# Optimization experiments

Hardware: AMD Instinct MI355X
Metric: run time of the kernel (lower is better)

The kernel has to match this reference:

```python
import jax, jax.numpy as jnp
import numpy as np

N = 100000
E = 1000000
C = 64      # hidden_channels
H = 4       # heads
O = C // H  # out channels per head
NEG_SLOPE = 0.2


def setup_inputs() -> dict:
    key = jax.random.key(0)
    ks = jax.random.split(key, 14)
    x = jax.random.normal(ks[0], (N, C), dtype=jnp.float32)
    edge_index = jax.random.randint(ks[1], (2, E), 0, N, dtype=jnp.int64)
    s = 1.0 / np.sqrt(C)
    params = {}
    for l in range(3):
        params[f"Wl{l+1}"] = jax.random.normal(ks[2 + 4 * l], (C, H * O), dtype=jnp.float32) * s
        params[f"Wr{l+1}"] = jax.random.normal(ks[3 + 4 * l], (C, H * O), dtype=jnp.float32) * s
        params[f"a{l+1}"] = jax.random.normal(ks[4 + 4 * l], (H, O), dtype=jnp.float32) * s
        params[f"b{l+1}"] = jnp.zeros((H * O,), dtype=jnp.float32)
    return {"x": x, "edge_index": edge_index, **params}


def _gatv2_layer(x, src, dst, Wl, Wr, a, b):
    # x: [N, C]; src/dst: [E]
    xl = (x @ Wl).reshape(N, H, O)  # source-side transform
    xr = (x @ Wr).reshape(N, H, O)  # target-side transform
    s = jax.nn.leaky_relu(xl[src] + xr[dst], NEG_SLOPE)     # [E, H, O]
    e = jnp.einsum("eho,ho->eh", s, a)                       # [E, H] logits
    # segment softmax over incoming edges of each target node
    m = jax.ops.segment_max(e, dst, num_segments=N)          # [N, H]
    ex = jnp.exp(e - m[dst])
    denom = jax.ops.segment_sum(ex, dst, num_segments=N)     # [N, H]
    alpha = ex / (denom[dst] + 1e-16)                        # [E, H]
    out = jax.ops.segment_sum(xl[src] * alpha[:, :, None], dst, num_segments=N)
    return out.reshape(N, H * O) + b


def reference(x, edge_index, Wl1, Wr1, a1, b1, Wl2, Wr2, a2, b2, Wl3, Wr3, a3, b3):
    src, dst = edge_index[0], edge_index[1]
    h = jax.nn.relu(_gatv2_layer(x, src, dst, Wl1, Wr1, a1, b1))
    h = jax.nn.relu(_gatv2_layer(h, src, dst, Wl2, Wr2, a2, b2))
    h = _gatv2_layer(h, src, dst, Wl3, Wr3, a3, b3)
    return h
```

## Files before the change

### kernel.cpp

```cpp
#include <hip/hip_runtime.h>
#include <hip/hip_fp16.h>
#include <math.h>

#define SLOPE 0.2f
#define LOG2E 1.4426950408889634f

#define DPP_ADD(x, ctrl) \
    ((x) + __int_as_float(__builtin_amdgcn_update_dpp( \
        0, __float_as_int(x), (ctrl), 0xF, 0xF, true)))


#define NPB 256
#define EPB 2048
#define MAXBK 2048

__global__ __launch_bounds__(256) void kH1(const int* __restrict__ ei,
                                           int* __restrict__ hist,
                                           int E, int nbk, int nblkE) {
    __shared__ int h[MAXBK];
    int t = threadIdx.x, b = blockIdx.x;
    for (int i = t; i < nbk; i += 256) h[i] = 0;
    __syncthreads();
    int e0 = b * EPB, e1 = min(e0 + EPB, E);
    for (int e = e0 + t; e < e1; e += 256)
        atomicAdd(&h[ei[E + e] >> 8], 1);
    __syncthreads();
    for (int i = t; i < nbk; i += 256)
        hist[i * nblkE + b] = h[i];
}

__global__ __launch_bounds__(256) void k_scan1(const int* __restrict__ deg,
                                               int* __restrict__ rp,
                                               int* __restrict__ blk, int n) {
    __shared__ int sd[256];
    int t = threadIdx.x;
    int base = blockIdx.x * 1024 + t * 4;
    int v0 = 0, v1 = 0, v2 = 0, v3 = 0;
    if (base + 0 < n) v0 = deg[base + 0];
    if (base + 1 < n) v1 = deg[base + 1];
    if (base + 2 < n) v2 = deg[base + 2];
    if (base + 3 < n) v3 = deg[base + 3];
    int s = v0 + v1 + v2 + v3;
    sd[t] = s;
    __syncthreads();
    for (int off = 1; off < 256; off <<= 1) {
        int x = (t >= off) ? sd[t - off] : 0;
        __syncthreads();
        sd[t] += x;
        __syncthreads();
    }
    int ex = sd[t] - s;
    if (t == 255) blk[blockIdx.x] = sd[255];
    if (base + 0 < n) rp[base + 0] = ex; ex += v0;
    if (base + 1 < n) rp[base + 1] = ex; ex += v1;
    if (base + 2 < n) rp[base + 2] = ex; ex += v2;
    if (base + 3 < n) rp[base + 3] = ex;
}

__global__ __launch_bounds__(256) void k_scan3(int* __restrict__ rp,
                                               const int* __restrict__ blk,
                                               int n) {
    __shared__ int red[256];
    int t = threadIdx.x, b = blockIdx.x;
    int v = 0;
    for (int i = t; i < b; i += 256) v += blk[i];
    red[t] = v;
    __syncthreads();
    for (int off = 128; off; off >>= 1) {
        if (t < off) red[t] += red[t + off];
        __syncthreads();
    }
    int off0 = red[0];
    int base = b * 1024 + t * 4;
    #pragma unroll
    for (int i = 0; i < 4; i++) {
        int idx = base + i;
        if (idx < n) rp[idx] += off0;
    }
}

__global__ __launch_bounds__(256) void kH2(const int* __restrict__ ei,
                                           const int* __restrict__ hs,
                                           int* __restrict__ pairs,
                                           int E, int nbk, int nblkE) {
    __shared__ int soff[MAXBK];
    int t = threadIdx.x, b = blockIdx.x;
    for (int i = t; i < nbk; i += 256) soff[i] = hs[i * nblkE + b];
    __syncthreads();
    int e0 = b * EPB, e1 = min(e0 + EPB, E);
    for (int e = e0 + t; e < e1; e += 256) {
        int s = ei[e], d = ei[E + e];
        int slot = atomicAdd(&soff[d >> 8], 1);
        pairs[slot] = (s << 8) | (d & (NPB - 1));
    }
}

__global__ __launch_bounds__(256) void kB3(const int* __restrict__ hs,
                                           const int* __restrict__ pairs,
                                           int* __restrict__ btot,
                                           int E, int nbk, int nblkE) {
    __shared__ int sdeg[NPB];
    __shared__ int red[256];
    int t = threadIdx.x, b = blockIdx.x;
    sdeg[t] = 0;
    __syncthreads();
    int s0 = hs[b * nblkE];
    int s1 = (b + 1 < nbk) ? hs[(b + 1) * nblkE] : E;
    for (int i = s0 + t; i < s1; i += 256)
        atomicAdd(&sdeg[pairs[i] & (NPB - 1)], 1);
    __syncthreads();
    red[t] = (sdeg[t] + 15) & ~15;
    __syncthreads();
    for (int off = 128; off; off >>= 1) {
        if (t < off) red[t] += red[t + off];
        __syncthreads();
    }
    if (t == 0) btot[b] = red[0];
}

__global__ __launch_bounds__(256) void kB4(const int* __restrict__ hs,
                                           const int* __restrict__ pairs,
                                           const int* __restrict__ btot,
                                           int* __restrict__ rp,
                                           int* __restrict__ deg,
                                           int* __restrict__ col,
                                           int E, int nbk, int nblkE, int n) {
    __shared__ int sdeg[NPB];
    __shared__ int spfx[NPB];
    int t = threadIdx.x, b = blockIdx.x;

    int v = 0;
    for (int i = t; i < b; i += 256) v += btot[i];
    spfx[t] = v;
    __syncthreads();
    for (int off = 128; off; off >>= 1) {
        if (t < off) spfx[t] += spfx[t + off];
        __syncthreads();
    }
    int bb = spfx[0];
    __syncthreads();

    sdeg[t] = 0;
    __syncthreads();
    int s0 = hs[b * nblkE];
    int s1 = (b + 1 < nbk) ? hs[(b + 1) * nblkE] : E;
    for (int i = s0 + t; i < s1; i += 256)
        atomicAdd(&sdeg[pairs[i] & (NPB - 1)], 1);
    __syncthreads();
    int cnt = sdeg[t];
    int pv = (cnt + 15) & ~15;
    spfx[t] = pv;
    __syncthreads();
    for (int off = 1; off < 256; off <<= 1) {
        int x = (t >= off) ? spfx[t - off] : 0;
        __syncthreads();
        spfx[t] += x;
        __syncthreads();
    }
    int rpt = bb + spfx[t] - pv;
    int node = b * NPB + t;
    if (node < n) { rp[node] = rpt; deg[node] = cnt; }
    __syncthreads();
    sdeg[t] = rpt;
    __syncthreads();
    for (int i = s0 + t; i < s1; i += 256) {
        int p = pairs[i];
        int slot = atomicAdd(&sdeg[p & (NPB - 1)], 1);
        col[slot] = (p & ~(NPB - 1)) >> 1;
    }
    if (node < n)
        for (int i = rpt + cnt; i < rpt + pv; i++) col[i] = 0;
}


__global__ __launch_bounds__(512) void k_gemm(const float* __restrict__ in,
                                              const float* __restrict__ Wl,
                                              const float* __restrict__ Wr,
                                              __half* __restrict__ xl,
                                              __half* __restrict__ xr, int n) {
    __shared__ float4 sW[64 * 32];
    __shared__ float  sx[128 * 68];

    int t = threadIdx.x;
    int base = blockIdx.x * 128;

    float4 xs[4];
    int xrow[4], xkq[4];
    #pragma unroll
    for (int s = 0; s < 4; s++) {
        int i = t + 512 * s;
        int row = i >> 4, kq = i & 15;
        int g = base + row;
        if (g > n - 1) g = n - 1;
        xs[s] = *(const float4*)(in + (size_t)g * 64 + kq * 4);
        xrow[s] = row; xkq[s] = kq;
    }
    for (int i = t; i < 2048; i += 512) {
        int k = i >> 5, jg = i & 31;
        const float* src = (jg < 16) ? (Wl + k * 64 + jg * 4)
                                     : (Wr + k * 64 + (jg - 16) * 4);
        sW[i] = *(const float4*)src;
    }
    #pragma unroll
    for (int s = 0; s < 4; s++)
        *(float4*)(sx + xrow[s] * 68 + xkq[s] * 4) = xs[s];
    __syncthreads();

    int rt = t & 31;
    int ct = t >> 5;
    const float* sxp = sx + rt * 68;

    float4 acc[4][2];
    #pragma unroll
    for (int r = 0; r < 4; r++)
        #pragma unroll
        for (int j = 0; j < 2; j++) acc[r][j] = make_float4(0.f, 0.f, 0.f, 0.f);

    #pragma unroll 1
    for (int k0 = 0; k0 < 64; k0 += 4) {
        float4 xv[4];
        #pragma unroll
        for (int r = 0; r < 4; r++)
            xv[r] = *(const float4*)(sxp + r * (32 * 68) + k0);
        #pragma unroll
        for (int kk = 0; kk < 4; kk++) {
            float4 w0 = sW[(k0 + kk) * 32 + ct * 2 + 0];
            float4 w1 = sW[(k0 + kk) * 32 + ct * 2 + 1];
            #pragma unroll
            for (int r = 0; r < 4; r++) {
                float xk = (kk == 0) ? xv[r].x : (kk == 1) ? xv[r].y
                         : (kk == 2) ? xv[r].z : xv[r].w;
                acc[r][0].x += xk * w0.x;
                acc[r][0].y += xk * w0.y;
                acc[r][0].z += xk * w0.z;
                acc[r][0].w += xk * w0.w;
                acc[r][1].x += xk * w1.x;
                acc[r][1].y += xk * w1.y;
                acc[r][1].z += xk * w1.z;
                acc[r][1].w += xk * w1.w;
            }
        }
    }

    __half* outh = (ct < 8) ? xl : xr;
    int cq = (ct & 7) * 8;
    #pragma unroll
    for (int r = 0; r < 4; r++) {
        int g = base + rt + 32 * r;
        if (g < n) {
            union { int4 i4; __half2 h[4]; } u;
            u.h[0] = __floats2half2_rn(acc[r][0].x, acc[r][0].y);
            u.h[1] = __floats2half2_rn(acc[r][0].z, acc[r][0].w);
            u.h[2] = __floats2half2_rn(acc[r][1].x, acc[r][1].y);
            u.h[3] = __floats2half2_rn(acc[r][1].z, acc[r][1].w);
            *(int4*)(outh + (size_t)g * 64 + cq) = u.i4;
        }
    }
}


__global__ __launch_bounds__(256) void k_node(const __half* __restrict__ xl,
                                              const __half* __restrict__ xr,
                                              const int* __restrict__ rp,
                                              const int* __restrict__ deg,
                                              const int* __restrict__ col,
                                              const float* __restrict__ A,
                                              const float* __restrict__ Bv,
                                              float* __restrict__ outp,
                                              int n, int relu) {
    int lane = threadIdx.x & 63;
    int node = __builtin_amdgcn_readfirstlane(blockIdx.x * 4 + (threadIdx.x >> 6));
    if (node >= n) return;
    int grp = lane >> 5;
    int s   = lane & 31;
    int chn = ((s >> 3) << 4) + ((s & 7) << 1);
    unsigned cofs = (unsigned)chn * 2u;

    float2 xr2 = __half22float2(*(const __half2*)(xr + (size_t)node * 64 + chn));
    float2 a2  = *(const float2*)(A + chn);
    a2.x *= LOG2E; a2.y *= LOG2E;
    float2 b2  = *(const float2*)(Bv + chn);

    int start = rp[node];
    int d = deg[node];
    int nb = (d + 7) >> 3;
    const int* cp = col + start;
    const char* xlb = (const char*)xl;

    float den = 0.f;
    float ax = 0.f, ay = 0.f;

    auto batch = [&](const float2 (&v)[4], int ebase, bool full) {
        #pragma unroll
        for (int j = 0; j < 4; j++) {
            float sx_ = v[j].x + xr2.x;
            float sy_ = v[j].y + xr2.y;
            sx_ = fmaxf(sx_, SLOPE * sx_);
            sy_ = fmaxf(sy_, SLOPE * sy_);
            float q = sx_ * a2.x + sy_ * a2.y;
            q = DPP_ADD(q, 0xB1);
            q = DPP_ADD(q, 0x4E);
            q = DPP_ADD(q, 0x141);
            if (!full) {
                int eidx = ebase + 2 * j + grp;
                if (eidx >= d) q = -INFINITY;
            }
            float w = __builtin_amdgcn_exp2f(q);
            den += w;
            ax += w * v[j].x;
            ay += w * v[j].y;
        }
    };

    auto gather = [&](float2 (&v)[4], const int* q) {
        int c[8];
        *(int4*)(c + 0) = *(const int4*)(q + 0);
        *(int4*)(c + 4) = *(const int4*)(q + 4);
        #pragma unroll
        for (int j = 0; j < 4; j++) {
            unsigned cc = (unsigned)(grp ? c[2 * j + 1] : c[2 * j]);
            v[j] = __half22float2(*(const __half2*)(xlb + (cc + cofs)));
        }
    };

    float2 v[4];
    if (nb > 0) gather(v, cp);

    #pragma unroll 1
    for (int b = 0; b < nb - 1; b++) {
        float2 vN[4];
        gather(vN, cp + (b + 1) * 8);
        batch(v, b * 8, true);
        #pragma unroll
        for (int j = 0; j < 4; j++) v[j] = vN[j];
    }
    if (nb > 0) batch(v, (nb - 1) * 8, false);

    den += __shfl_xor(den, 32, 64);
    ax  += __shfl_xor(ax, 32, 64);
    ay  += __shfl_xor(ay, 32, 64);

    float inv = 1.f / (den + 1e-16f);
    float ox = ax * inv + b2.x;
    float oy = ay * inv + b2.y;
    if (relu) { ox = fmaxf(ox, 0.f); oy = fmaxf(oy, 0.f); }
    if (grp == 0)
        *(float2*)(outp + (size_t)node * 64 + chn) = make_float2(ox, oy);
}


extern "C" void kernel_launch(void* const* d_in, const int* in_sizes, int n_in,
                              void* d_out, int out_size, void* d_ws, size_t ws_size,
                              hipStream_t stream) {
    const float* x = (const float*)d_in[0];
    const int* ei = (const int*)d_in[1];
    int N = in_sizes[0] / 64;
    int E = in_sizes[1] / 2;

    const float* Wl[3] = {(const float*)d_in[2], (const float*)d_in[6], (const float*)d_in[10]};
    const float* Wr[3] = {(const float*)d_in[3], (const float*)d_in[7], (const float*)d_in[11]};
    const float* Av[3] = {(const float*)d_in[4], (const float*)d_in[8], (const float*)d_in[12]};
    const float* Bv[3] = {(const float*)d_in[5], (const float*)d_in[9], (const float*)d_in[13]};

    char* w = (char*)d_ws;
    auto carve = [&](size_t bytes) {
        void* p = (void*)w;
        w += (bytes + 255) & ~(size_t)255;
        return p;
    };
    int NBK    = (N + NPB - 1) / NPB;
    int NBLK_E = (E + EPB - 1) / EPB;
    size_t histN = (size_t)NBK * NBLK_E;
    size_t colN = (size_t)E + 15 * (size_t)N + 64;
    __half* xl   = (__half*)carve((size_t)N * 64 * 2);
    __half* xr   = (__half*)carve((size_t)N * 64 * 2);
    float* h     = (float*)carve((size_t)N * 64 * 4);
    int*   rp    = (int*)carve((size_t)N * 4);
    int*   deg   = (int*)carve((size_t)N * 4);
    int*   col   = (int*)carve(colN * 4);
    int*   pairs = (int*)carve((size_t)E * 4);
    int*   hist  = (int*)carve(histN * 4);
    int*   hs    = (int*)carve(histN * 4);
    int*   btot  = (int*)carve((size_t)NBK * 4);
    int*   blkB  = (int*)carve(512 * 4);

    int nblkH1024 = (int)((histN + 1023) / 1024);
    int gemm_grid = (N + 127) / 128;
    int node_grid = (N + 3) / 4;

    kH1<<<NBLK_E, 256, 0, stream>>>(ei, hist, E, NBK, NBLK_E);
    k_scan1<<<nblkH1024, 256, 0, stream>>>(hist, hs, blkB, (int)histN);
    k_scan3<<<nblkH1024, 256, 0, stream>>>(hs, blkB, (int)histN);
    kH2<<<NBLK_E, 256, 0, stream>>>(ei, hs, pairs, E, NBK, NBLK_E);

    kB3<<<NBK, 256, 0, stream>>>(hs, pairs, btot, E, NBK, NBLK_E);
    kB4<<<NBK, 256, 0, stream>>>(hs, pairs, btot, rp, deg, col, E, NBK, NBLK_E, N);

    const float* in_l = x;
    for (int l = 0; l < 3; l++) {
        float* out_l = (l == 2) ? (float*)d_out : h;
        int relu = (l < 2) ? 1 : 0;
        k_gemm<<<gemm_grid, 512, 0, stream>>>(in_l, Wl[l], Wr[l], xl, xr, N);
        k_node<<<node_grid, 256, 0, stream>>>(xl, xr, rp, deg, col, Av[l], Bv[l],
                                              out_l, N, relu);
        in_l = h;
    }
}
```

Measured before the change: 325.9 us.

## Fuse node aggregation with next layer's GEMM via shared memory

Adds a k_fused kernel that runs the edge-softmax aggregation for 128 nodes per block, applies bias and ReLU, keeps the 64-channel result in shared memory, and then multiplies it by the next layer's Wl and Wr to write the fp16 xl and xr directly. Layers 1 and 2 use this kernel with ping-pong buffers, so the fp32 hidden tensor is never written to or read back from global memory and two launches are dropped. The cost is lower parallelism per block: each wave now handles 16 nodes one after another with half-wave edge batches, where k_node used many small blocks, and the larger shared-memory footprint may reduce occupancy.

```diff
diff --git a/kernel.cpp b/kernel.cpp
--- a/kernel.cpp
+++ b/kernel.cpp
@@ -243,6 +243,166 @@
     }
 
     __half* outh = (ct < 8) ? xl : xr;
+    int cq = (ct & 7) * 8;
+    #pragma unroll
+    for (int r = 0; r < 4; r++) {
+        int g = base + rt + 32 * r;
+        if (g < n) {
+            union { int4 i4; __half2 h[4]; } u;
+            u.h[0] = __floats2half2_rn(acc[r][0].x, acc[r][0].y);
+            u.h[1] = __floats2half2_rn(acc[r][0].z, acc[r][0].w);
+            u.h[2] = __floats2half2_rn(acc[r][1].x, acc[r][1].y);
+            u.h[3] = __floats2half2_rn(acc[r][1].z, acc[r][1].w);
+            *(int4*)(outh + (size_t)g * 64 + cq) = u.i4;
+        }
+    }
+}
+
+
+__global__ __launch_bounds__(512) void k_fused(const __half* __restrict__ xli,
+                                               const __half* __restrict__ xri,
+                                               const int* __restrict__ rp,
+                                               const int* __restrict__ deg,
+                                               const int* __restrict__ col,
+                                               const float* __restrict__ A,
+                                               const float* __restrict__ Bv,
+                                               const float* __restrict__ Wl,
+                                               const float* __restrict__ Wr,
+                                               __half* __restrict__ xlo,
+                                               __half* __restrict__ xro,
+                                               int n) {
+    __shared__ float4 sW[64 * 32];
+    __shared__ float  sx[128 * 68];
+
+    int t = threadIdx.x;
+    int base = blockIdx.x * 128;
+
+    for (int i = t; i < 2048; i += 512) {
+        int k = i >> 5, jg = i & 31;
+        const float* src = (jg < 16) ? (Wl + k * 64 + jg * 4)
+                                     : (Wr + k * 64 + (jg - 16) * 4);
+        sW[i] = *(const float4*)src;
+    }
+
+    int lane = t & 63;
+    int wv = t >> 6;
+    int grp = lane >> 5;
+    int s = lane & 31;
+    int chn = ((s >> 3) << 4) + ((s & 7) << 1);
+    unsigned cofs = (unsigned)chn * 2u;
+    float2 a2 = *(const float2*)(A + chn);
+    a2.x *= LOG2E; a2.y *= LOG2E;
+    float2 b2 = *(const float2*)(Bv + chn);
+    const char* xlb = (const char*)xli;
+
+    #pragma unroll 1
+    for (int ni = 0; ni < 16; ni++) {
+        int local = wv * 16 + ni;
+        int node = __builtin_amdgcn_readfirstlane(base + local);
+        if (node >= n) break;
+
+        float2 xr2 = __half22float2(
+            *(const __half2*)(xri + (size_t)node * 64 + chn));
+        int start = rp[node];
+        int d = deg[node];
+        int nb = (d + 7) >> 3;
+        const int* cp = col + start;
+
+        float den = 0.f, ax = 0.f, ay = 0.f;
+
+        auto batch = [&](const float2 (&v)[4], int ebase, bool full) {
+            #pragma unroll
+            for (int j = 0; j < 4; j++) {
+                float sx_ = v[j].x + xr2.x;
+                float sy_ = v[j].y + xr2.y;
+                sx_ = fmaxf(sx_, SLOPE * sx_);
+                sy_ = fmaxf(sy_, SLOPE * sy_);
+                float q = sx_ * a2.x + sy_ * a2.y;
+                q = DPP_ADD(q, 0xB1);
+                q = DPP_ADD(q, 0x4E);
+                q = DPP_ADD(q, 0x141);
+                if (!full) {
+                    int eidx = ebase + 2 * j + grp;
+                    if (eidx >= d) q = -INFINITY;
+                }
+                float w = __builtin_amdgcn_exp2f(q);
+                den += w;
+                ax += w * v[j].x;
+                ay += w * v[j].y;
+            }
+        };
+        auto gather = [&](float2 (&v)[4], const int* q) {
+            int c[8];
+            *(int4*)(c + 0) = *(const int4*)(q + 0);
+            *(int4*)(c + 4) = *(const int4*)(q + 4);
+            #pragma unroll
+            for (int j = 0; j < 4; j++) {
+                unsigned cc = (unsigned)(grp ? c[2 * j + 1] : c[2 * j]);
+                v[j] = __half22float2(*(const __half2*)(xlb + (cc + cofs)));
+            }
+        };
+
+        float2 v[4];
+        if (nb > 0) gather(v, cp);
+        #pragma unroll 1
+        for (int b = 0; b < nb - 1; b++) {
+            float2 vN[4];
+            gather(vN, cp + (b + 1) * 8);
+            batch(v, b * 8, true);
+            #pragma unroll
+            for (int j = 0; j < 4; j++) v[j] = vN[j];
+        }
+        if (nb > 0) batch(v, (nb - 1) * 8, false);
+
+        den += __shfl_xor(den, 32, 64);
+        ax  += __shfl_xor(ax, 32, 64);
+        ay  += __shfl_xor(ay, 32, 64);
+
+        float inv = 1.f / (den + 1e-16f);
+        float ox = fmaxf(ax * inv + b2.x, 0.f);
+        float oy = fmaxf(ay * inv + b2.y, 0.f);
+        if (grp == 0)
+            *(float2*)(sx + local * 68 + chn) = make_float2(ox, oy);
+    }
+    __syncthreads();
+
+    int rt = t & 31;
+    int ct = t >> 5;
+    const float* sxp = sx + rt * 68;
+
+    float4 acc[4][2];
+    #pragma unroll
+    for (int r = 0; r < 4; r++)
+        #pragma unroll
+        for (int j = 0; j < 2; j++) acc[r][j] = make_float4(0.f, 0.f, 0.f, 0.f);
+
+    #pragma unroll 1
+    for (int k0 = 0; k0 < 64; k0 += 4) {
+        float4 xv[4];
+        #pragma unroll
+        for (int r = 0; r < 4; r++)
+            xv[r] = *(const float4*)(sxp + r * (32 * 68) + k0);
+        #pragma unroll
+        for (int kk = 0; kk < 4; kk++) {
+            float4 w0 = sW[(k0 + kk) * 32 + ct * 2 + 0];
+            float4 w1 = sW[(k0 + kk) * 32 + ct * 2 + 1];
+            #pragma unroll
+            for (int r = 0; r < 4; r++) {
+                float xk = (kk == 0) ? xv[r].x : (kk == 1) ? xv[r].y
+                         : (kk == 2) ? xv[r].z : xv[r].w;
+                acc[r][0].x += xk * w0.x;
+                acc[r][0].y += xk * w0.y;
+                acc[r][0].z += xk * w0.z;
+                acc[r][0].w += xk * w0.w;
+                acc[r][1].x += xk * w1.x;
+                acc[r][1].y += xk * w1.y;
+                acc[r][1].z += xk * w1.z;
+                acc[r][1].w += xk * w1.w;
+            }
+        }
+    }
+
+    __half* outh = (ct < 8) ? xlo : xro;
     int cq = (ct & 7) * 8;
     #pragma unroll
     for (int r = 0; r < 4; r++) {
@@ -372,9 +532,10 @@
     int NBLK_E = (E + EPB - 1) / EPB;
     size_t histN = (size_t)NBK * NBLK_E;
     size_t colN = (size_t)E + 15 * (size_t)N + 64;
-    __half* xl   = (__half*)carve((size_t)N * 64 * 2);
-    __half* xr   = (__half*)carve((size_t)N * 64 * 2);
-    float* h     = (float*)carve((size_t)N * 64 * 4);
+    __half* xlA  = (__half*)carve((size_t)N * 64 * 2);
+    __half* xrA  = (__half*)carve((size_t)N * 64 * 2);
+    __half* xlB  = (__half*)carve((size_t)N * 64 * 2);
+    __half* xrB  = (__half*)carve((size_t)N * 64 * 2);
     int*   rp    = (int*)carve((size_t)N * 4);
     int*   deg   = (int*)carve((size_t)N * 4);
     int*   col   = (int*)carve(colN * 4);
@@ -385,8 +546,9 @@
     int*   blkB  = (int*)carve(512 * 4);
 
     int nblkH1024 = (int)((histN + 1023) / 1024);
-    int gemm_grid = (N + 127) / 128;
-    int node_grid = (N + 3) / 4;
+    int gemm_grid  = (N + 127) / 128;
+    int fused_grid = (N + 127) / 128;
+    int node_grid  = (N + 3) / 4;
 
     kH1<<<NBLK_E, 256, 0, stream>>>(ei, hist, E, NBK, NBLK_E);
     k_scan1<<<nblkH1024, 256, 0, stream>>>(hist, hs, blkB, (int)histN);
@@ -396,13 +558,13 @@
     kB3<<<NBK, 256, 0, stream>>>(hs, pairs, btot, E, NBK, NBLK_E);
     kB4<<<NBK, 256, 0, stream>>>(hs, pairs, btot, rp, deg, col, E, NBK, NBLK_E, N);
 
-    const float* in_l = x;
-    for (int l = 0; l < 3; l++) {
-        float* out_l = (l == 2) ? (float*)d_out : h;
-        int relu = (l < 2) ? 1 : 0;
-        k_gemm<<<gemm_grid, 512, 0, stream>>>(in_l, Wl[l], Wr[l], xl, xr, N);
-        k_node<<<node_grid, 256, 0, stream>>>(xl, xr, rp, deg, col, Av[l], Bv[l],
-                                              out_l, N, relu);
-        in_l = h;
-    }
-}
+    k_gemm<<<gemm_grid, 512, 0, stream>>>(x, Wl[0], Wr[0], xlA, xrA, N);
+    k_fused<<<fused_grid, 512, 0, stream>>>(xlA, xrA, rp, deg, col,
+                                            Av[0], Bv[0], Wl[1], Wr[1],
+                                            xlB, xrB, N);
+    k_fused<<<fused_grid, 512, 0, stream>>>(xlB, xrB, rp, deg, col,
+                                            Av[1], Bv[1], Wl[2], Wr[2],
+                                            xlA, xrA, N);
+    k_node<<<node_grid, 256, 0, stream>>>(xlA, xrA, rp, deg, col, Av[2], Bv[2],
+                                          (float*)d_out, N, 0);
+}
```

New measurement: 351.3 us. +7.8%, slower.
